# Kernel optimization log

Measured on AMD Instinct MI355X. Metric: run time of the kernel, lower is better.

The kernel has to match this reference:

```python
import jax, jax.numpy as jnp
import numpy as np

TOP_K = 2


def setup_inputs() -> dict:
    key = jax.random.key(0)
    ks = jax.random.split(key, 5)
    B, S, H, E, F = 2, 4096, 2048, 8, 4096
    scale_h = 1.0 / np.sqrt(H)
    scale_f = 1.0 / np.sqrt(F)
    return {
        "hidden_states": jax.random.normal(ks[0], (B, S, H), jnp.float32),
        "gate_w": jax.random.normal(ks[1], (E, H), jnp.float32) * scale_h,
        "w1": jax.random.normal(ks[2], (E, F, H), jnp.float32) * scale_h,
        "w3": jax.random.normal(ks[3], (E, F, H), jnp.float32) * scale_h,
        "w2": jax.random.normal(ks[4], (E, H, F), jnp.float32) * scale_f,
    }


def reference(hidden_states, gate_w, w1, w3, w2):
    B, S, H = hidden_states.shape
    E = gate_w.shape[0]
    x = hidden_states.reshape(-1, H)                      # [T, H]
    T = x.shape[0]

    # Router: logits -> softmax(fp32) -> top-k -> renormalize
    router_logits = x @ gate_w.T                          # [T, E]
    probs = jax.nn.softmax(router_logits.astype(jnp.float32), axis=-1)
    topk_w, topk_idx = jax.lax.top_k(probs, TOP_K)        # [T, k]
    topk_w = topk_w / jnp.sum(topk_w, axis=-1, keepdims=True)
    topk_w = topk_w.astype(x.dtype)

    # Per-expert combine weight (0 for unselected experts) [T, E]
    combine = jnp.sum(jax.nn.one_hot(topk_idx, E, dtype=x.dtype)
                      * topk_w[..., None], axis=1)

    # Expert SwiGLU MLPs, weighted-accumulated (loop over fixed E=8)
    out = jnp.zeros((T, H), dtype=x.dtype)
    for e in range(E):
        h = jax.nn.silu(x @ w1[e].T) * (x @ w3[e].T)      # [T, F]
        out = out + (h @ w2[e].T) * combine[:, e:e + 1]   # [T, H]

    return out.reshape(B, S, H), router_logits
```

## Files before the change

kernel.cpp:

```cpp
#include <hip/hip_runtime.h>
#include <math.h>

#define T_TOK 8192
#define H_DIM 2048
#define F_DIM 4096
#define E_NUM 8
#define MAXPAIR (T_TOK * 2)
#define MAX_MT 136
#define BM 128
#define BN 128
#define BK 32
#define NCONV 2048
#define NCONV13 4096

typedef __attribute__((ext_vector_type(4))) float f32x4;
typedef __attribute__((ext_vector_type(8))) short s16x8;
typedef __attribute__((ext_vector_type(8))) __bf16 bf16x8;
typedef __attribute__((ext_vector_type(4))) unsigned short u16x4;

__device__ __forceinline__ unsigned short f2bf(float f) {
  unsigned int u = __float_as_uint(f);
  u += 0x7FFFu + ((u >> 16) & 1u);
  return (unsigned short)(u >> 16);
}

__device__ __forceinline__ s16x8 pack8(f32x4 a, f32x4 b) {
  s16x8 r;
  r[0] = (short)f2bf(a.x); r[1] = (short)f2bf(a.y);
  r[2] = (short)f2bf(a.z); r[3] = (short)f2bf(a.w);
  r[4] = (short)f2bf(b.x); r[5] = (short)f2bf(b.y);
  r[6] = (short)f2bf(b.z); r[7] = (short)f2bf(b.w);
  return r;
}

#define GLD16(gsrc, ldst)                                                      \
  __builtin_amdgcn_global_load_lds(                                            \
      (__attribute__((address_space(1))) void*)(gsrc),                         \
      (__attribute__((address_space(3))) void*)(ldst), 16, 0, 0)

__global__ __launch_bounds__(256) void router_conv_kernel(
    const float* __restrict__ x, const float* __restrict__ gw,
    float* __restrict__ logits, unsigned short* __restrict__ xb,
    int* __restrict__ ctrl, int* __restrict__ tIdx, float* __restrict__ tW,
    const float* __restrict__ w1f, unsigned short* __restrict__ w1b,
    const float* __restrict__ w3f, unsigned short* __restrict__ w3b,
    int nconv) {
  int rb = blockIdx.x;
  if (nconv) {
    const int bid = blockIdx.x;
    if ((bid % 3) != 2) {
      const int cid = bid - (bid + 1) / 3;
      const float* src = (cid < 2048) ? w1f : w3f;
      unsigned short* dst = (cid < 2048) ? w1b : w3b;
      const long long base = (long long)(cid & 2047) * 4096;
#pragma unroll
      for (int it = 0; it < 16; ++it) {
        const long long i = base + it * 256 + threadIdx.x;
        f32x4 a = *(const f32x4*)(src + i * 8);
        f32x4 b = *(const f32x4*)(src + i * 8 + 4);
        *(s16x8*)(dst + i * 8) = pack8(a, b);
      }
      return;
    }
    rb = bid / 3;
  }

  const int wid = threadIdx.x >> 6, lane = threadIdx.x & 63;
  const int t = rb * 4 + wid;
  const float* xr = x + (size_t)t * H_DIM;
  float acc[E_NUM];
#pragma unroll
  for (int e = 0; e < E_NUM; ++e) acc[e] = 0.f;
#pragma unroll
  for (int c = 0; c < H_DIM / 256; ++c) {
    const int h0 = c * 256 + lane * 4;
    f32x4 xv = *(const f32x4*)(xr + h0);
    u16x4 p;
    p.x = f2bf(xv.x); p.y = f2bf(xv.y); p.z = f2bf(xv.z); p.w = f2bf(xv.w);
    *(u16x4*)(xb + (size_t)t * H_DIM + h0) = p;
#pragma unroll
    for (int e = 0; e < E_NUM; ++e) {
      f32x4 gv = *(const f32x4*)(gw + (size_t)e * H_DIM + h0);
      acc[e] += xv.x * gv.x + xv.y * gv.y + xv.z * gv.z + xv.w * gv.w;
    }
  }
#pragma unroll
  for (int e = 0; e < E_NUM; ++e) {
#pragma unroll
    for (int off = 32; off >= 1; off >>= 1) acc[e] += __shfl_xor(acc[e], off, 64);
  }
  if (lane == 0) {
#pragma unroll
    for (int e = 0; e < E_NUM; ++e) logits[(size_t)t * E_NUM + e] = acc[e];
    int i0 = 0;
    float m0 = acc[0];
    for (int e = 1; e < E_NUM; ++e)
      if (acc[e] > m0) { m0 = acc[e]; i0 = e; }
    int i1 = -1;
    float m1 = -3.4e38f;
    for (int e = 0; e < E_NUM; ++e)
      if (e != i0 && acc[e] > m1) { m1 = acc[e]; i1 = e; }
    float ex = expf(m1 - m0);
    float w0 = 1.f / (1.f + ex);
    float w1 = ex * w0;
    tIdx[t * 2] = i0; tIdx[t * 2 + 1] = i1;
    tW[t * 2] = w0;  tW[t * 2 + 1] = w1;
    atomicAdd(&ctrl[i0], 1);
    atomicAdd(&ctrl[i1], 1);
  }
}

__global__ __launch_bounds__(256) void plan_kernel(int* __restrict__ ctrl) {
  __shared__ int cnt[E_NUM], offs[E_NUM + 1], tbase[E_NUM + 1];
  const int t = threadIdx.x;
  if (t < E_NUM) cnt[t] = ctrl[t];
  __syncthreads();
  if (t == 0) {
    int off = 0, mt = 0;
    for (int e = 0; e < E_NUM; ++e) {
      offs[e] = off; tbase[e] = mt;
      ctrl[8 + e] = off;
      ctrl[16 + e] = off;
      off += cnt[e];
      mt += (cnt[e] + BM - 1) / BM;
    }
    offs[E_NUM] = off; tbase[E_NUM] = mt;
    ctrl[24] = mt;
  }
  __syncthreads();
  const int total = tbase[E_NUM];
  for (int i = t; i < total; i += 256) {
    int e = 0;
    while (tbase[e + 1] <= i) ++e;
    ctrl[32 + i] = e;
    ctrl[32 + MAX_MT + i] = offs[e] + (i - tbase[e]) * BM;
  }
}

__global__ __launch_bounds__(256) void scatter_kernel(
    const int* __restrict__ tIdx, const float* __restrict__ tW,
    int* __restrict__ ctrl, int* __restrict__ pairTok,
    float* __restrict__ pairWgt) {
  const int t = blockIdx.x * 256 + threadIdx.x;
  if (t >= T_TOK) return;
#pragma unroll
  for (int j = 0; j < 2; ++j) {
    const int e = tIdx[t * 2 + j];
    const int pos = atomicAdd(&ctrl[16 + e], 1);
    pairTok[pos] = t;
    pairWgt[pos] = tW[t * 2 + j];
  }
}

template <int BBF>
__global__ __launch_bounds__(256, 2) void gemm1_kernel(
    const float* __restrict__ w1f, const float* __restrict__ w3f,
    const unsigned short* __restrict__ w1b,
    const unsigned short* __restrict__ w3b,
    const unsigned short* __restrict__ xb, const int* __restrict__ ctrl,
    const int* __restrict__ pairTok, unsigned short* __restrict__ hbuf,
    const float* __restrict__ w2f, unsigned short* __restrict__ w2b,
    int nconv) {
  int gid = blockIdx.x;
  const int nconv3 = nconv * 3;
  if (gid < nconv3) {
    if ((gid % 3) == 2) {
      const int cid = gid / 3;
      const long long per = (long long)E_NUM * F_DIM * H_DIM / 8 / NCONV;
      long long i = (long long)cid * per + threadIdx.x;
      const long long end = (long long)(cid + 1) * per;
      for (; i < end; i += 256) {
        f32x4 a = *(const f32x4*)(w2f + i * 8);
        f32x4 b = *(const f32x4*)(w2f + i * 8 + 4);
        *(s16x8*)(w2b + i * 8) = pack8(a, b);
      }
      return;
    }
    gid = gid - (gid + 1) / 3;
  } else {
    gid = gid - nconv;
  }

  const int mtTotal = ctrl[24];
  const int mt = gid >> 5;
  const int nt = gid & 31;
  if (mt >= mtTotal) return;
  const int e = ctrl[32 + mt];
  const int mbase = ctrl[32 + MAX_MT + mt];
  int mValid = ctrl[8 + e] + ctrl[e] - mbase;
  if (mValid > BM) mValid = BM;
  const int nbase = nt * BN;

  __shared__ __align__(16) short sA[3][BM * BK];
  __shared__ __align__(16) short sB1[3][BM * BK];
  __shared__ __align__(16) short sB3[3][BM * BK];
  __shared__ int sTok[BM];

  const int tid = threadIdx.x;
  if (tid < BM) sTok[tid] = pairTok[mbase + (tid < mValid ? tid : 0)];
  __syncthreads();

  const int c0 = tid, c1 = tid + 256;
  const int r0 = c0 >> 2, r1 = c1 >> 2;
  const int kg0 = (c0 & 3) ^ ((r0 >> 1) & 3);
  const int kg1 = (c1 & 3) ^ ((r1 >> 1) & 3);

  const unsigned short* srcA0 = xb + (size_t)sTok[r0] * H_DIM + kg0 * 8;
  const unsigned short* srcA1 = xb + (size_t)sTok[r1] * H_DIM + kg1 * 8;
  const size_t wbase = (size_t)e * F_DIM * H_DIM;
  const float *f10, *f11, *f30, *f31;
  const unsigned short *p10, *p11, *p30, *p31;
  if constexpr (BBF) {
    p10 = w1b + wbase + (size_t)(nbase + r0) * H_DIM + kg0 * 8;
    p11 = w1b + wbase + (size_t)(nbase + r1) * H_DIM + kg1 * 8;
    p30 = w3b + wbase + (size_t)(nbase + r0) * H_DIM + kg0 * 8;
    p31 = w3b + wbase + (size_t)(nbase + r1) * H_DIM + kg1 * 8;
  } else {
    f10 = w1f + wbase + (size_t)(nbase + r0) * H_DIM + kg0 * 8;
    f11 = w1f + wbase + (size_t)(nbase + r1) * H_DIM + kg1 * 8;
    f30 = w3f + wbase + (size_t)(nbase + r0) * H_DIM + kg0 * 8;
    f31 = w3f + wbase + (size_t)(nbase + r1) * H_DIM + kg1 * 8;
  }

  f32x4 acc1[4][4], acc3[4][4];
  const f32x4 fz = {0.f, 0.f, 0.f, 0.f};
#pragma unroll
  for (int i = 0; i < 4; ++i)
#pragma unroll
    for (int j = 0; j < 4; ++j) { acc1[i][j] = fz; acc3[i][j] = fz; }

  const int lane = tid & 63, wid = tid >> 6;
  const int wm = (wid >> 1) * 64, wn = (wid & 1) * 64;
  const int rl = lane & 15, kq = lane >> 4;

  int aIdx[4], bIdx[4];
#pragma unroll
  for (int i = 0; i < 4; ++i) {
    const int ra = wm + i * 16 + rl;
    aIdx[i] = ra * BK + ((kq ^ ((ra >> 1) & 3)) * 8);
    const int rb = wn + i * 16 + rl;
    bIdx[i] = rb * BK + ((kq ^ ((rb >> 1) & 3)) * 8);
  }

#define STAGE1(buf, k0)                                                        \
  {                                                                            \
    GLD16(srcA0 + (k0), &sA[buf][c0 * 8]);                                     \
    GLD16(srcA1 + (k0), &sA[buf][c1 * 8]);                                     \
    if constexpr (BBF) {                                                       \
      GLD16(p10 + (k0), &sB1[buf][c0 * 8]);                                    \
      GLD16(p11 + (k0), &sB1[buf][c1 * 8]);                                    \
      GLD16(p30 + (k0), &sB3[buf][c0 * 8]);                                    \
      GLD16(p31 + (k0), &sB3[buf][c1 * 8]);                                    \
    } else {                                                                   \
      f32x4 t0 = *(const f32x4*)(f10 + (k0));                                  \
      f32x4 t1 = *(const f32x4*)(f10 + (k0) + 4);                              \
      *(s16x8*)&sB1[buf][c0 * 8] = pack8(t0, t1);                              \
      t0 = *(const f32x4*)(f11 + (k0));                                        \
      t1 = *(const f32x4*)(f11 + (k0) + 4);                                    \
      *(s16x8*)&sB1[buf][c1 * 8] = pack8(t0, t1);                              \
      t0 = *(const f32x4*)(f30 + (k0));                                        \
      t1 = *(const f32x4*)(f30 + (k0) + 4);                                    \
      *(s16x8*)&sB3[buf][c0 * 8] = pack8(t0, t1);                              \
      t0 = *(const f32x4*)(f31 + (k0));                                        \
      t1 = *(const f32x4*)(f31 + (k0) + 4);                                    \
      *(s16x8*)&sB3[buf][c1 * 8] = pack8(t0, t1);                              \
    }                                                                          \
  }

  STAGE1(0, 0);
  STAGE1(1, BK);
  if constexpr (BBF)
    asm volatile("s_waitcnt vmcnt(6)" ::: "memory");
  else
    asm volatile("s_waitcnt vmcnt(0) lgkmcnt(0)" ::: "memory");
  __builtin_amdgcn_s_barrier();
  asm volatile("" ::: "memory");

  const int NS = H_DIM / BK;
  int cur = 0;
  for (int s = 0; s < NS; ++s) {
    if (s + 2 < NS) {
      const int nxt = (cur + 2 >= 3) ? cur - 1 : cur + 2;
      STAGE1(nxt, (s + 2) * BK);
    }
    asm volatile("" ::: "memory");

    bf16x8 af[4], bf1[4], bf3[4];
#pragma unroll
    for (int i = 0; i < 4; ++i) {
      af[i] = *(const bf16x8*)&sA[cur][aIdx[i]];
      bf1[i] = *(const bf16x8*)&sB1[cur][bIdx[i]];
      bf3[i] = *(const bf16x8*)&sB3[cur][bIdx[i]];
    }
    __builtin_amdgcn_s_setprio(1);
#pragma unroll
    for (int mr = 0; mr < 4; ++mr)
#pragma unroll
      for (int nr = 0; nr < 4; ++nr) {
        acc1[mr][nr] = __builtin_amdgcn_mfma_f32_16x16x32_bf16(
            af[mr], bf1[nr], acc1[mr][nr], 0, 0, 0);
        acc3[mr][nr] = __builtin_amdgcn_mfma_f32_16x16x32_bf16(
            af[mr], bf3[nr], acc3[mr][nr], 0, 0, 0);
      }
    __builtin_amdgcn_s_setprio(0);
    asm volatile("" ::: "memory");

    if (s + 1 < NS) {
      if constexpr (BBF) {
        if (s + 2 < NS)
          asm volatile("s_waitcnt vmcnt(6)" ::: "memory");
        else
          asm volatile("s_waitcnt vmcnt(0)" ::: "memory");
      } else {
        asm volatile("s_waitcnt vmcnt(0) lgkmcnt(0)" ::: "memory");
      }
      __builtin_amdgcn_s_barrier();
      asm volatile("" ::: "memory");
    }
    cur = (cur + 1 >= 3) ? 0 : cur + 1;
  }

#pragma unroll
  for (int mr = 0; mr < 4; ++mr) {
#pragma unroll
    for (int j = 0; j < 4; ++j) {
      const int row = wm + mr * 16 + kq * 4 + j;
      if (row < mValid) {
        unsigned short* dst =
            hbuf + (size_t)(mbase + row) * F_DIM + nbase + wn + rl;
#pragma unroll
        for (int nr = 0; nr < 4; ++nr) {
          const float z = acc1[mr][nr][j];
          const float hv = (z / (1.f + expf(-z))) * acc3[mr][nr][j];
          dst[nr * 16] = f2bf(hv);
        }
      }
    }
  }
#undef STAGE1
}

template <int BBF>
__global__ __launch_bounds__(256, 2) void gemm2_kernel(
    const float* __restrict__ w2f, const unsigned short* __restrict__ w2b,
    const unsigned short* __restrict__ hbuf, const int* __restrict__ ctrl,
    const int* __restrict__ pairTok, const float* __restrict__ pairWgt,
    float* __restrict__ out) {
  const int mtTotal = ctrl[24];
  const int mt = blockIdx.x >> 4;
  const int nt = blockIdx.x & 15;
  if (mt >= mtTotal) return;
  const int e = ctrl[32 + mt];
  const int mbase = ctrl[32 + MAX_MT + mt];
  int mValid = ctrl[8 + e] + ctrl[e] - mbase;
  if (mValid > BM) mValid = BM;
  const int nbase = nt * BN;

  __shared__ __align__(16) short sA[3][BM * BK];
  __shared__ __align__(16) short sB[3][BM * BK];
  __shared__ int sTok[BM];
  __shared__ float sWgt[BM];

  const int tid = threadIdx.x;
  if (tid < BM) {
    const int p = mbase + (tid < mValid ? tid : 0);
    sTok[tid] = pairTok[p];
    sWgt[tid] = pairWgt[p];
  }
  __syncthreads();

  const int c0 = tid, c1 = tid + 256;
  const int r0 = c0 >> 2, r1 = c1 >> 2;
  const int kg0 = (c0 & 3) ^ ((r0 >> 1) & 3);
  const int kg1 = (c1 & 3) ^ ((r1 >> 1) & 3);

  size_t pa0 = (size_t)(mbase + r0); if (pa0 > MAXPAIR - 1) pa0 = MAXPAIR - 1;
  size_t pa1 = (size_t)(mbase + r1); if (pa1 > MAXPAIR - 1) pa1 = MAXPAIR - 1;
  const unsigned short* srcA0 = hbuf + pa0 * F_DIM + kg0 * 8;
  const unsigned short* srcA1 = hbuf + pa1 * F_DIM + kg1 * 8;
  const size_t wbase = (size_t)e * H_DIM * F_DIM;
  const float *fw0, *fw1;
  const unsigned short *pw0, *pw1;
  if constexpr (BBF) {
    pw0 = w2b + wbase + (size_t)(nbase + r0) * F_DIM + kg0 * 8;
    pw1 = w2b + wbase + (size_t)(nbase + r1) * F_DIM + kg1 * 8;
  } else {
    fw0 = w2f + wbase + (size_t)(nbase + r0) * F_DIM + kg0 * 8;
    fw1 = w2f + wbase + (size_t)(nbase + r1) * F_DIM + kg1 * 8;
  }

  f32x4 acc[4][4];
  const f32x4 fz = {0.f, 0.f, 0.f, 0.f};
#pragma unroll
  for (int i = 0; i < 4; ++i)
#pragma unroll
    for (int j = 0; j < 4; ++j) acc[i][j] = fz;

  const int lane = tid & 63, wid = tid >> 6;
  const int wm = (wid >> 1) * 64, wn = (wid & 1) * 64;
  const int rl = lane & 15, kq = lane >> 4;

  int aIdx[4], bIdx[4];
#pragma unroll
  for (int i = 0; i < 4; ++i) {
    const int ra = wm + i * 16 + rl;
    aIdx[i] = ra * BK + ((kq ^ ((ra >> 1) & 3)) * 8);
    const int rb = wn + i * 16 + rl;
    bIdx[i] = rb * BK + ((kq ^ ((rb >> 1) & 3)) * 8);
  }

#define STAGE2(buf, k0)                                                        \
  {                                                                            \
    GLD16(srcA0 + (k0), &sA[buf][c0 * 8]);                                     \
    GLD16(srcA1 + (k0), &sA[buf][c1 * 8]);                                     \
    if constexpr (BBF) {                                                       \
      GLD16(pw0 + (k0), &sB[buf][c0 * 8]);                                     \
      GLD16(pw1 + (k0), &sB[buf][c1 * 8]);                                     \
    } else {                                                                   \
      f32x4 t0 = *(const f32x4*)(fw0 + (k0));                                  \
      f32x4 t1 = *(const f32x4*)(fw0 + (k0) + 4);                              \
      *(s16x8*)&sB[buf][c0 * 8] = pack8(t0, t1);                               \
      t0 = *(const f32x4*)(fw1 + (k0));                                        \
      t1 = *(const f32x4*)(fw1 + (k0) + 4);                                    \
      *(s16x8*)&sB[buf][c1 * 8] = pack8(t0, t1);                               \
    }                                                                          \
  }

  STAGE2(0, 0);
  STAGE2(1, BK);
  if constexpr (BBF)
    asm volatile("s_waitcnt vmcnt(4)" ::: "memory");
  else
    asm volatile("s_waitcnt vmcnt(0) lgkmcnt(0)" ::: "memory");
  __builtin_amdgcn_s_barrier();
  asm volatile("" ::: "memory");

  const int NS = F_DIM / BK;
  int cur = 0;
  for (int s = 0; s < NS; ++s) {
    if (s + 2 < NS) {
      const int nxt = (cur + 2 >= 3) ? cur - 1 : cur + 2;
      STAGE2(nxt, (s + 2) * BK);
    }
    asm volatile("" ::: "memory");

    bf16x8 af[4], bf[4];
#pragma unroll
    for (int i = 0; i < 4; ++i) {
      af[i] = *(const bf16x8*)&sA[cur][aIdx[i]];
      bf[i] = *(const bf16x8*)&sB[cur][bIdx[i]];
    }
    __builtin_amdgcn_s_setprio(1);
#pragma unroll
    for (int mr = 0; mr < 4; ++mr)
#pragma unroll
      for (int nr = 0; nr < 4; ++nr)
        acc[mr][nr] = __builtin_amdgcn_mfma_f32_16x16x32_bf16(
            af[mr], bf[nr], acc[mr][nr], 0, 0, 0);
    __builtin_amdgcn_s_setprio(0);
    asm volatile("" ::: "memory");

    if (s + 1 < NS) {
      if constexpr (BBF) {
        if (s + 2 < NS)
          asm volatile("s_waitcnt vmcnt(4)" ::: "memory");
        else
          asm volatile("s_waitcnt vmcnt(0)" ::: "memory");
      } else {
        asm volatile("s_waitcnt vmcnt(0) lgkmcnt(0)" ::: "memory");
      }
      __builtin_amdgcn_s_barrier();
      asm volatile("" ::: "memory");
    }
    cur = (cur + 1 >= 3) ? 0 : cur + 1;
  }

#pragma unroll
  for (int mr = 0; mr < 4; ++mr) {
#pragma unroll
    for (int j = 0; j < 4; ++j) {
      const int row = wm + mr * 16 + kq * 4 + j;
      if (row < mValid) {
        const int tok = sTok[row];
        const float w = sWgt[row];
        float* dst = out + (size_t)tok * H_DIM + nbase + wn + rl;
#pragma unroll
        for (int nr = 0; nr < 4; ++nr)
          unsafeAtomicAdd(dst + nr * 16, w * acc[mr][nr][j]);
      }
    }
  }
#undef STAGE2
}

extern "C" void kernel_launch(void* const* d_in, const int* in_sizes, int n_in,
                              void* d_out, int out_size, void* d_ws,
                              size_t ws_size, hipStream_t stream) {
  const float* x  = (const float*)d_in[0];
  const float* gw = (const float*)d_in[1];
  const float* w1 = (const float*)d_in[2];
  const float* w3 = (const float*)d_in[3];
  const float* w2 = (const float*)d_in[4];
  float* out = (float*)d_out;
  float* logits = out + (size_t)T_TOK * H_DIM;

  char* ws = (char*)d_ws;
  const size_t HDR = 1u << 20;
  const size_t XB_SZ = (size_t)T_TOK * H_DIM * 2;
  const size_t HB_SZ = (size_t)MAXPAIR * F_DIM * 2;
  const size_t W_SZ  = (size_t)E_NUM * F_DIM * H_DIM * 2;

  int* ctrl = (int*)(ws);
  int* tIdx = (int*)(ws + 4096);
  float* tW = (float*)(ws + 4096 + 65536);
  int* pairTok = (int*)(ws + 4096 + 131072);
  float* pairWgt = (float*)(ws + 4096 + 196608);
  unsigned short* xb = (unsigned short*)(ws + HDR);
  unsigned short* hbuf = (unsigned short*)(ws + HDR + XB_SZ);
  unsigned short* w1b = (unsigned short*)(ws + HDR + XB_SZ + HB_SZ);
  unsigned short* w3b = w1b + W_SZ / 2;
  unsigned short* w2b = w3b + W_SZ / 2;

  const bool cw13 = ws_size >= HDR + XB_SZ + HB_SZ + 2 * W_SZ;
  const bool cw2  = ws_size >= HDR + XB_SZ + HB_SZ + 3 * W_SZ;

  hipMemsetAsync(ctrl, 0, 4096, stream);
  hipMemsetAsync(out, 0, (size_t)T_TOK * H_DIM * sizeof(float), stream);

  if (cw13)
    router_conv_kernel<<<6144, 256, 0, stream>>>(
        x, gw, logits, xb, ctrl, tIdx, tW, w1, w1b, w3, w3b, NCONV13);
  else
    router_conv_kernel<<<T_TOK / 4, 256, 0, stream>>>(
        x, gw, logits, xb, ctrl, tIdx, tW, w1, w1b, w3, w3b, 0);

  plan_kernel<<<1, 256, 0, stream>>>(ctrl);
  scatter_kernel<<<T_TOK / 256, 256, 0, stream>>>(tIdx, tW, ctrl, pairTok, pairWgt);

  const int NG = MAX_MT * 32;
  if (cw13) {
    const int nconv = cw2 ? NCONV : 0;
    gemm1_kernel<1><<<NG + nconv, 256, 0, stream>>>(
        w1, w3, w1b, w3b, xb, ctrl, pairTok, hbuf, w2, w2b, nconv);
  } else {
    gemm1_kernel<0><<<NG, 256, 0, stream>>>(
        w1, w3, w1b, w3b, xb, ctrl, pairTok, hbuf, w2, w2b, 0);
  }
  if (cw2)
    gemm2_kernel<1><<<MAX_MT * 16, 256, 0, stream>>>(w2, w2b, hbuf, ctrl,
                                                     pairTok, pairWgt, out);
  else
    gemm2_kernel<0><<<MAX_MT * 16, 256, 0, stream>>>(w2, w2b, hbuf, ctrl,
                                                     pairTok, pairWgt, out);
}
```

Before: 1.435 ms.

## Use 256-row M tiles in down-projection GEMM with separate tile plan

The down-projection GEMM moves from 128x128 to 256x128 tiles. Each wave now computes 64x128 with 32 accumulators, and the planner builds a second expert tile map at 256-row granularity. This halves how often the w2 weight tile is re-fetched per expert and cuts the number of blocks. In exchange it raises register and LDS pressure, which can lower occupancy, and adds more padding waste for experts with partial tiles.

```diff
diff --git a/kernel.cpp b/kernel.cpp
--- a/kernel.cpp
+++ b/kernel.cpp
@@ -7,7 +7,9 @@
 #define E_NUM 8
 #define MAXPAIR (T_TOK * 2)
 #define MAX_MT 136
+#define MAX_MT2 80
 #define BM 128
+#define BM2 256
 #define BN 128
 #define BK 32
 #define NCONV 2048
@@ -111,29 +113,36 @@
 }
 
 __global__ __launch_bounds__(256) void plan_kernel(int* __restrict__ ctrl) {
-  __shared__ int cnt[E_NUM], offs[E_NUM + 1], tbase[E_NUM + 1];
+  __shared__ int cnt[E_NUM], offs[E_NUM + 1], tb1[E_NUM + 1], tb2[E_NUM + 1];
   const int t = threadIdx.x;
   if (t < E_NUM) cnt[t] = ctrl[t];
   __syncthreads();
   if (t == 0) {
-    int off = 0, mt = 0;
+    int off = 0, mt = 0, mt2 = 0;
     for (int e = 0; e < E_NUM; ++e) {
-      offs[e] = off; tbase[e] = mt;
+      offs[e] = off; tb1[e] = mt; tb2[e] = mt2;
       ctrl[8 + e] = off;
       ctrl[16 + e] = off;
+      mt += (cnt[e] + BM - 1) / BM;
+      mt2 += (cnt[e] + BM2 - 1) / BM2;
       off += cnt[e];
-      mt += (cnt[e] + BM - 1) / BM;
-    }
-    offs[E_NUM] = off; tbase[E_NUM] = mt;
+    }
+    offs[E_NUM] = off; tb1[E_NUM] = mt; tb2[E_NUM] = mt2;
     ctrl[24] = mt;
+    ctrl[25] = mt2;
   }
   __syncthreads();
-  const int total = tbase[E_NUM];
-  for (int i = t; i < total; i += 256) {
+  for (int i = t; i < tb1[E_NUM]; i += 256) {
     int e = 0;
-    while (tbase[e + 1] <= i) ++e;
+    while (tb1[e + 1] <= i) ++e;
     ctrl[32 + i] = e;
-    ctrl[32 + MAX_MT + i] = offs[e] + (i - tbase[e]) * BM;
+    ctrl[168 + i] = offs[e] + (i - tb1[e]) * BM;
+  }
+  for (int i = t; i < tb2[E_NUM]; i += 256) {
+    int e = 0;
+    while (tb2[e + 1] <= i) ++e;
+    ctrl[304 + i] = e;
+    ctrl[384 + i] = offs[e] + (i - tb2[e]) * BM2;
   }
 }
 
@@ -186,7 +195,7 @@
   const int nt = gid & 31;
   if (mt >= mtTotal) return;
   const int e = ctrl[32 + mt];
-  const int mbase = ctrl[32 + MAX_MT + mt];
+  const int mbase = ctrl[168 + mt];
   int mValid = ctrl[8 + e] + ctrl[e] - mbase;
   if (mValid > BM) mValid = BM;
   const int nbase = nt * BN;
@@ -346,38 +355,43 @@
     const unsigned short* __restrict__ hbuf, const int* __restrict__ ctrl,
     const int* __restrict__ pairTok, const float* __restrict__ pairWgt,
     float* __restrict__ out) {
-  const int mtTotal = ctrl[24];
+  const int mtTotal = ctrl[25];
   const int mt = blockIdx.x >> 4;
   const int nt = blockIdx.x & 15;
   if (mt >= mtTotal) return;
-  const int e = ctrl[32 + mt];
-  const int mbase = ctrl[32 + MAX_MT + mt];
+  const int e = ctrl[304 + mt];
+  const int mbase = ctrl[384 + mt];
   int mValid = ctrl[8 + e] + ctrl[e] - mbase;
-  if (mValid > BM) mValid = BM;
+  if (mValid > BM2) mValid = BM2;
   const int nbase = nt * BN;
 
-  __shared__ __align__(16) short sA[3][BM * BK];
-  __shared__ __align__(16) short sB[3][BM * BK];
-  __shared__ int sTok[BM];
-  __shared__ float sWgt[BM];
+  __shared__ __align__(16) short sA[3][BM2 * BK];
+  __shared__ __align__(16) short sB[3][BN * BK];
+  __shared__ int sTok[BM2];
+  __shared__ float sWgt[BM2];
 
   const int tid = threadIdx.x;
-  if (tid < BM) {
+  {
     const int p = mbase + (tid < mValid ? tid : 0);
     sTok[tid] = pairTok[p];
     sWgt[tid] = pairWgt[p];
   }
   __syncthreads();
 
+  const unsigned short* srcA[4];
+#pragma unroll
+  for (int j = 0; j < 4; ++j) {
+    const int c = tid + j * 256;
+    const int row = c >> 2;
+    const int kg = (c & 3) ^ ((row >> 1) & 3);
+    size_t p = (size_t)(mbase + row);
+    if (p > MAXPAIR - 1) p = MAXPAIR - 1;
+    srcA[j] = hbuf + p * F_DIM + kg * 8;
+  }
   const int c0 = tid, c1 = tid + 256;
   const int r0 = c0 >> 2, r1 = c1 >> 2;
   const int kg0 = (c0 & 3) ^ ((r0 >> 1) & 3);
   const int kg1 = (c1 & 3) ^ ((r1 >> 1) & 3);
-
-  size_t pa0 = (size_t)(mbase + r0); if (pa0 > MAXPAIR - 1) pa0 = MAXPAIR - 1;
-  size_t pa1 = (size_t)(mbase + r1); if (pa1 > MAXPAIR - 1) pa1 = MAXPAIR - 1;
-  const unsigned short* srcA0 = hbuf + pa0 * F_DIM + kg0 * 8;
-  const unsigned short* srcA1 = hbuf + pa1 * F_DIM + kg1 * 8;
   const size_t wbase = (size_t)e * H_DIM * F_DIM;
   const float *fw0, *fw1;
   const unsigned short *pw0, *pw1;
@@ -389,30 +403,33 @@
     fw1 = w2f + wbase + (size_t)(nbase + r1) * F_DIM + kg1 * 8;
   }
 
-  f32x4 acc[4][4];
+  f32x4 acc[4][8];
   const f32x4 fz = {0.f, 0.f, 0.f, 0.f};
 #pragma unroll
   for (int i = 0; i < 4; ++i)
 #pragma unroll
-    for (int j = 0; j < 4; ++j) acc[i][j] = fz;
+    for (int j = 0; j < 8; ++j) acc[i][j] = fz;
 
   const int lane = tid & 63, wid = tid >> 6;
-  const int wm = (wid >> 1) * 64, wn = (wid & 1) * 64;
+  const int wm = wid * 64;
   const int rl = lane & 15, kq = lane >> 4;
 
-  int aIdx[4], bIdx[4];
+  int aIdx[4], bIdx[8];
 #pragma unroll
   for (int i = 0; i < 4; ++i) {
     const int ra = wm + i * 16 + rl;
     aIdx[i] = ra * BK + ((kq ^ ((ra >> 1) & 3)) * 8);
-    const int rb = wn + i * 16 + rl;
+  }
+#pragma unroll
+  for (int i = 0; i < 8; ++i) {
+    const int rb = i * 16 + rl;
     bIdx[i] = rb * BK + ((kq ^ ((rb >> 1) & 3)) * 8);
   }
 
 #define STAGE2(buf, k0)                                                        \
   {                                                                            \
-    GLD16(srcA0 + (k0), &sA[buf][c0 * 8]);                                     \
-    GLD16(srcA1 + (k0), &sA[buf][c1 * 8]);                                     \
+    _Pragma("unroll") for (int j = 0; j < 4; ++j)                              \
+        GLD16(srcA[j] + (k0), &sA[buf][(tid + j * 256) * 8]);                  \
     if constexpr (BBF) {                                                       \
       GLD16(pw0 + (k0), &sB[buf][c0 * 8]);                                     \
       GLD16(pw1 + (k0), &sB[buf][c1 * 8]);                                     \
@@ -429,7 +446,7 @@
   STAGE2(0, 0);
   STAGE2(1, BK);
   if constexpr (BBF)
-    asm volatile("s_waitcnt vmcnt(4)" ::: "memory");
+    asm volatile("s_waitcnt vmcnt(6)" ::: "memory");
   else
     asm volatile("s_waitcnt vmcnt(0) lgkmcnt(0)" ::: "memory");
   __builtin_amdgcn_s_barrier();
@@ -444,17 +461,16 @@
     }
     asm volatile("" ::: "memory");
 
-    bf16x8 af[4], bf[4];
-#pragma unroll
-    for (int i = 0; i < 4; ++i) {
-      af[i] = *(const bf16x8*)&sA[cur][aIdx[i]];
-      bf[i] = *(const bf16x8*)&sB[cur][bIdx[i]];
-    }
+    bf16x8 af[4], bf[8];
+#pragma unroll
+    for (int i = 0; i < 4; ++i) af[i] = *(const bf16x8*)&sA[cur][aIdx[i]];
+#pragma unroll
+    for (int i = 0; i < 8; ++i) bf[i] = *(const bf16x8*)&sB[cur][bIdx[i]];
     __builtin_amdgcn_s_setprio(1);
 #pragma unroll
     for (int mr = 0; mr < 4; ++mr)
 #pragma unroll
-      for (int nr = 0; nr < 4; ++nr)
+      for (int nr = 0; nr < 8; ++nr)
         acc[mr][nr] = __builtin_amdgcn_mfma_f32_16x16x32_bf16(
             af[mr], bf[nr], acc[mr][nr], 0, 0, 0);
     __builtin_amdgcn_s_setprio(0);
@@ -463,7 +479,7 @@
     if (s + 1 < NS) {
       if constexpr (BBF) {
         if (s + 2 < NS)
-          asm volatile("s_waitcnt vmcnt(4)" ::: "memory");
+          asm volatile("s_waitcnt vmcnt(6)" ::: "memory");
         else
           asm volatile("s_waitcnt vmcnt(0)" ::: "memory");
       } else {
@@ -483,9 +499,9 @@
       if (row < mValid) {
         const int tok = sTok[row];
         const float w = sWgt[row];
-        float* dst = out + (size_t)tok * H_DIM + nbase + wn + rl;
-#pragma unroll
-        for (int nr = 0; nr < 4; ++nr)
+        float* dst = out + (size_t)tok * H_DIM + nbase + rl;
+#pragma unroll
+        for (int nr = 0; nr < 8; ++nr)
           unsafeAtomicAdd(dst + nr * 16, w * acc[mr][nr][j]);
       }
     }
@@ -547,9 +563,9 @@
         w1, w3, w1b, w3b, xb, ctrl, pairTok, hbuf, w2, w2b, 0);
   }
   if (cw2)
-    gemm2_kernel<1><<<MAX_MT * 16, 256, 0, stream>>>(w2, w2b, hbuf, ctrl,
-                                                     pairTok, pairWgt, out);
+    gemm2_kernel<1><<<MAX_MT2 * 16, 256, 0, stream>>>(w2, w2b, hbuf, ctrl,
+                                                      pairTok, pairWgt, out);
   else
-    gemm2_kernel<0><<<MAX_MT * 16, 256, 0, stream>>>(w2, w2b, hbuf, ctrl,
-                                                     pairTok, pairWgt, out);
-}
+    gemm2_kernel<0><<<MAX_MT2 * 16, 256, 0, stream>>>(w2, w2b, hbuf, ctrl,
+                                                      pairTok, pairWgt, out);
+}
```

Measured after the change: 1.500 ms. +4.5%, slower.
